# Kernel optimization log

Hardware: AMD Instinct MI355X
Metric: run time of the kernel (lower is better)

Reference implementation:

```python
import jax, jax.numpy as jnp
import numpy as np

N_NODES = 100000
N_EDGES = 3200000
N_PAIRS = 500000
D_IN = 256
D_HID = 256
D_OUT = 2


def setup_inputs() -> dict:
    key = jax.random.key(0)
    ks = jax.random.split(key, 9)
    s1 = 1.0 / np.sqrt(D_IN)
    s2 = 1.0 / np.sqrt(D_HID)
    s3 = 1.0 / np.sqrt(2 * D_HID)
    return {
        "x": jax.random.normal(ks[0], (N_NODES, D_IN), jnp.float32),
        "edge_index": jax.random.randint(ks[1], (2, N_EDGES), 0, N_NODES, jnp.int64 if jax.config.jax_enable_x64 else jnp.int32),
        "index": jax.random.randint(ks[2], (N_PAIRS, 2), 0, N_NODES, jnp.int64 if jax.config.jax_enable_x64 else jnp.int32),
        "W1": jax.random.normal(ks[3], (D_HID, D_IN), jnp.float32) * s1,
        "b1": jnp.zeros((D_HID,), jnp.float32),
        "W2": jax.random.normal(ks[4], (D_HID, D_HID), jnp.float32) * s2,
        "b2": jnp.zeros((D_HID,), jnp.float32),
        "W3": jax.random.normal(ks[5], (D_OUT, 2 * D_HID), jnp.float32) * s3,
        "b3": jnp.zeros((D_OUT,), jnp.float32),
    }


def _gin_conv(x, edge_index, W, b):
    # PyG GINConv (eps=0): nn((1+eps)*x + sum_{j in N(i)} x_j)
    src, dst = edge_index[0], edge_index[1]
    agg = jax.ops.segment_sum(x[src], dst, num_segments=x.shape[0])  # [N, d]
    return (x + agg) @ W.T + b


def reference(x, edge_index, index, W1, b1, W2, b2, W3, b3):
    h = jax.nn.relu(_gin_conv(x, edge_index, W1, b1))   # [N, D_HID]
    h = jax.nn.relu(_gin_conv(h, edge_index, W2, b2))   # [N, D_HID]
    pair = jnp.concatenate((h[index[:, 0]], h[index[:, 1]]), axis=-1)  # [P, 2*D_HID]
    logits = pair @ W3.T + b3                            # [P, D_OUT]
    return jax.nn.log_softmax(logits, axis=1)
```

## Files before the change

### kernel.cpp

```cpp
#include <hip/hip_runtime.h>
#include <hip/hip_bf16.h>

constexpr int N_NODES = 100000;
constexpr int N_EDGES = 3200000;
constexpr int N_PAIRS = 500000;
constexpr int D       = 256;

using frag_ab = __attribute__((ext_vector_type(8))) short;
using frag_cd = __attribute__((ext_vector_type(4))) float;
typedef unsigned short ushort8 __attribute__((ext_vector_type(8)));

static __device__ __forceinline__ float b2f(unsigned short u) {
  return __uint_as_float(((unsigned)u) << 16);
}
static __device__ __forceinline__ unsigned short f2bf(float f) {
  unsigned u = __float_as_uint(f);
  unsigned r = (u + 0x7fff + ((u >> 16) & 1)) >> 16;
  return (unsigned short)r;
}

__global__ void zero_ints(int* __restrict__ p, int n) {
  int i = blockIdx.x * blockDim.x + threadIdx.x;
  if (i < n) p[i] = 0;
}

__global__ void f32_to_bf16(const float4* __restrict__ in, ushort4* __restrict__ out, int n4) {
  int i = blockIdx.x * blockDim.x + threadIdx.x;
  int stride = gridDim.x * blockDim.x;
  for (; i < n4; i += stride) {
    const float4 v = in[i];
    ushort4 o;
    o.x = f2bf(v.x); o.y = f2bf(v.y); o.z = f2bf(v.z); o.w = f2bf(v.w);
    out[i] = o;
  }
}

__global__ void hist_kernel(const int* __restrict__ ei, int* __restrict__ counts) {
  int i = blockIdx.x * blockDim.x + threadIdx.x;
  if (i < N_EDGES) atomicAdd(&counts[ei[N_EDGES + i]], 1);
}

__global__ __launch_bounds__(1024) void scan_kernel(const int* __restrict__ counts,
                                                    int* __restrict__ cursor, int n) {
  __shared__ int wsum[16];
  __shared__ int carry;
  const int t = threadIdx.x, lane = t & 63, w = t >> 6;
  if (t == 0) carry = 0;
  __syncthreads();
  for (int base = 0; base < n; base += 1024) {
    int v = (base + t < n) ? counts[base + t] : 0;
    int s = v;
#pragma unroll
    for (int off = 1; off < 64; off <<= 1) {
      int u = __shfl_up(s, off, 64);
      if (lane >= off) s += u;
    }
    if (lane == 63) wsum[w] = s;
    __syncthreads();
    if (t < 16) {
      int ws = wsum[t];
#pragma unroll
      for (int off = 1; off < 16; off <<= 1) {
        int u = __shfl_up(ws, off, 64);
        if (lane >= off) ws += u;
      }
      wsum[t] = ws;
    }
    __syncthreads();
    const int wpre = (w == 0) ? 0 : wsum[w - 1];
    if (base + t < n) cursor[base + t] = carry + wpre + s - v;
    __syncthreads();
    if (t == 0) carry += wsum[15];
    __syncthreads();
  }
}

constexpr int FILL_SEG = 4096;
__global__ __launch_bounds__(256) void fill_kernel(const int* __restrict__ ei,
                                                   int* __restrict__ cursor,
                                                   int* __restrict__ csr) {
  const int range = blockIdx.x & 7;
  const int seg   = blockIdx.x >> 3;
  const int base  = seg * FILL_SEG;
  const int lo = range * 12500, hi = lo + 12500;
#pragma unroll
  for (int j = 0; j < FILL_SEG / 256; ++j) {
    const int i = base + j * 256 + threadIdx.x;
    if (i < N_EDGES) {
      const int dst = ei[N_EDGES + i];
      if (dst >= lo && dst < hi) {
        const int pos = atomicAdd(&cursor[dst], 1);
        csr[pos] = ei[i];
      }
    }
  }
}

__global__ __launch_bounds__(256) void gather_agg_bf16(const ushort* __restrict__ x,
                                                       const int* __restrict__ csr,
                                                       const int* __restrict__ cursor_end,
                                                       const int* __restrict__ counts,
                                                       ushort* __restrict__ out) {
  const int node = blockIdx.x * 4 + (threadIdx.x >> 6);
  const int lane = threadIdx.x & 63;
  const int half = lane >> 5;
  const int fl   = lane & 31;
  if (node >= N_NODES) return;
  const int end = cursor_end[node];
  const int beg = end - counts[node];
  const size_t fo = (size_t)fl * 8;

  float acc[8];
#pragma unroll
  for (int j = 0; j < 8; ++j) acc[j] = 0.f;

  if (half == 0) {
    const ushort8 self = *reinterpret_cast<const ushort8*>(x + (size_t)node * D + fo);
#pragma unroll
    for (int j = 0; j < 8; ++j) acc[j] += b2f(self[j]);
  }

  int o = beg + half;
  for (; o + 6 < end; o += 8) {
    const int s0 = csr[o], s1 = csr[o + 2], s2 = csr[o + 4], s3 = csr[o + 6];
    const ushort8 v0 = *reinterpret_cast<const ushort8*>(x + (size_t)s0 * D + fo);
    const ushort8 v1 = *reinterpret_cast<const ushort8*>(x + (size_t)s1 * D + fo);
    const ushort8 v2 = *reinterpret_cast<const ushort8*>(x + (size_t)s2 * D + fo);
    const ushort8 v3 = *reinterpret_cast<const ushort8*>(x + (size_t)s3 * D + fo);
#pragma unroll
    for (int j = 0; j < 8; ++j)
      acc[j] += (b2f(v0[j]) + b2f(v1[j])) + (b2f(v2[j]) + b2f(v3[j]));
  }
  for (; o < end; o += 2) {
    const ushort8 v = *reinterpret_cast<const ushort8*>(x + (size_t)csr[o] * D + fo);
#pragma unroll
    for (int j = 0; j < 8; ++j) acc[j] += b2f(v[j]);
  }

#pragma unroll
  for (int j = 0; j < 8; ++j) acc[j] += __shfl_xor(acc[j], 32, 64);

  if (half == 0) {
    ushort8 ov;
#pragma unroll
    for (int j = 0; j < 8; ++j) ov[j] = f2bf(acc[j]);
    *reinterpret_cast<ushort8*>(out + (size_t)node * D + fo) = ov;
  }
}

__global__ __launch_bounds__(256) void gemm_mfma_bf16(const ushort* __restrict__ A,
                                                      const ushort* __restrict__ W,
                                                      const float* __restrict__ bias,
                                                      ushort* __restrict__ C,
                                                      int M) {
  __shared__ __align__(16) ushort As[64 * 256];
  __shared__ __align__(16) ushort Ws[64 * 256];

  const int t = threadIdx.x;
  const int w = t >> 6, l = t & 63;
  const int row0 = blockIdx.x * 64;
  const int col0 = blockIdx.y * 64;

  {
    const float4 zero4 = {0.f, 0.f, 0.f, 0.f};
#pragma unroll
    for (int i = 0; i < 8; ++i) {
      const int chunk = t + i * 256;
      const int r  = chunk >> 5;
      const int kb = (chunk & 31) << 4;
      const int swz = kb ^ ((r & 7) << 4);
      const int grow = row0 + r;
      float4 av = zero4;
      if (grow < M)
        av = *reinterpret_cast<const float4*>(
            reinterpret_cast<const char*>(A) + (size_t)grow * 512 + kb);
      *reinterpret_cast<float4*>(reinterpret_cast<char*>(As) + r * 512 + swz) = av;
      const float4 wv = *reinterpret_cast<const float4*>(
          reinterpret_cast<const char*>(W) + (size_t)(col0 + r) * 512 + kb);
      *reinterpret_cast<float4*>(reinterpret_cast<char*>(Ws) + r * 512 + swz) = wv;
    }
  }
  __syncthreads();

  const int g  = l >> 4;
  const int fr = l & 15;

  frag_cd acc[4];
#pragma unroll
  for (int c = 0; c < 4; ++c) {
    acc[c][0] = 0.f; acc[c][1] = 0.f; acc[c][2] = 0.f; acc[c][3] = 0.f;
  }

  const int arow = w * 16 + fr;
  const char* Asb = reinterpret_cast<const char*>(As);
  const char* Wsb = reinterpret_cast<const char*>(Ws);
#pragma unroll
  for (int ks = 0; ks < 8; ++ks) {
    const int kb = ks * 64 + g * 16;
    const frag_ab af = *reinterpret_cast<const frag_ab*>(
        Asb + arow * 512 + (kb ^ ((arow & 7) << 4)));
#pragma unroll
    for (int c = 0; c < 4; ++c) {
      const int wrow = c * 16 + fr;
      const frag_ab bf = *reinterpret_cast<const frag_ab*>(
          Wsb + wrow * 512 + (kb ^ ((wrow & 7) << 4)));
      acc[c] = __builtin_amdgcn_mfma_f32_16x16x32_bf16(af, bf, acc[c], 0, 0, 0);
    }
  }
  __syncthreads();

  ushort* Ct = As;
#pragma unroll
  for (int c = 0; c < 4; ++c) {
    const int col = c * 16 + fr;
    const float bv = bias[col0 + col];
#pragma unroll
    for (int r = 0; r < 4; ++r) {
      const int rl = w * 16 + g * 4 + r;
      Ct[rl * 64 + col] = f2bf(fmaxf(acc[c][r] + bv, 0.f));
    }
  }
  __syncthreads();
#pragma unroll
  for (int i = 0; i < 2; ++i) {
    const int chunk = t + i * 256;
    const int r  = chunk >> 3;
    const int cb = (chunk & 7) << 4;
    const int grow = row0 + r;
    if (grow < M)
      *reinterpret_cast<float4*>(reinterpret_cast<char*>(C) + (size_t)grow * 512 + col0 * 2 + cb) =
          *reinterpret_cast<const float4*>(reinterpret_cast<const char*>(Ct) + r * 128 + cb);
  }
}

__global__ __launch_bounds__(256) void pair_head_bf16(const ushort* __restrict__ h,
                                                      const int* __restrict__ idx,
                                                      const float* __restrict__ W3,
                                                      const float* __restrict__ b3,
                                                      float* __restrict__ out) {
  const int wave = (int)((blockIdx.x * (size_t)blockDim.x + threadIdx.x) >> 6);
  const int lane = threadIdx.x & 63;
  const int half = lane >> 5;
  const int fl   = lane & 31;
  const int p0 = 2 * wave, p1 = 2 * wave + 1;
  if (p0 >= N_PAIRS) return;

  const int ia = idx[2 * p0 + half];
  const int ib = idx[2 * p1 + half];
  const ushort8 va = *reinterpret_cast<const ushort8*>(h + (size_t)ia * D + fl * 8);
  const ushort8 vb = *reinterpret_cast<const ushort8*>(h + (size_t)ib * D + fl * 8);

  const float4 w0a = *reinterpret_cast<const float4*>(W3 + lane * 8);
  const float4 w0b = *reinterpret_cast<const float4*>(W3 + lane * 8 + 4);
  const float4 w1a = *reinterpret_cast<const float4*>(W3 + 512 + lane * 8);
  const float4 w1b = *reinterpret_cast<const float4*>(W3 + 512 + lane * 8 + 4);
  const float w0[8] = {w0a.x, w0a.y, w0a.z, w0a.w, w0b.x, w0b.y, w0b.z, w0b.w};
  const float w1[8] = {w1a.x, w1a.y, w1a.z, w1a.w, w1b.x, w1b.y, w1b.z, w1b.w};

  float l00 = 0.f, l01 = 0.f, l10 = 0.f, l11 = 0.f;
#pragma unroll
  for (int j = 0; j < 8; ++j) {
    const float fa = b2f(va[j]), fb = b2f(vb[j]);
    l00 += fa * w0[j]; l01 += fa * w1[j];
    l10 += fb * w0[j]; l11 += fb * w1[j];
  }
#pragma unroll
  for (int off = 32; off > 0; off >>= 1) {
    l00 += __shfl_down(l00, off, 64);
    l01 += __shfl_down(l01, off, 64);
    l10 += __shfl_down(l10, off, 64);
    l11 += __shfl_down(l11, off, 64);
  }
  if (lane == 0) {
    const float bb0 = b3[0], bb1 = b3[1];
    l00 += bb0; l01 += bb1; l10 += bb0; l11 += bb1;
    const float m0 = fmaxf(l00, l01);
    const float lse0 = m0 + logf(expf(l00 - m0) + expf(l01 - m0));
    const float m1 = fmaxf(l10, l11);
    const float lse1 = m1 + logf(expf(l10 - m1) + expf(l11 - m1));
    float4 o;
    o.x = l00 - lse0; o.y = l01 - lse0; o.z = l10 - lse1; o.w = l11 - lse1;
    *reinterpret_cast<float4*>(out + 4 * (size_t)wave) = o;
  }
}

extern "C" void kernel_launch(void* const* d_in, const int* in_sizes, int n_in,
                              void* d_out, int out_size, void* d_ws, size_t ws_size,
                              hipStream_t stream) {
  const float* x   = (const float*)d_in[0];
  const int*   ei  = (const int*)d_in[1];
  const int*   idx = (const int*)d_in[2];
  const float* W1  = (const float*)d_in[3];
  const float* b1  = (const float*)d_in[4];
  const float* W2  = (const float*)d_in[5];
  const float* b2  = (const float*)d_in[6];
  const float* W3  = (const float*)d_in[7];
  const float* b3  = (const float*)d_in[8];
  float* out = (float*)d_out;

  const size_t feat = (size_t)N_NODES * D;
  char* ws = (char*)d_ws;
  ushort* xb    = (ushort*)(ws);
  ushort* aggb  = (ushort*)(ws + 51200000);
  ushort* hb    = (ushort*)(ws + 102400000);
  ushort* W1b   = (ushort*)(ws + 153600000);
  ushort* W2b   = (ushort*)(ws + 153731072);
  int* counts   = (int*)(ws + 153862144);
  int* cursor   = (int*)(ws + 154262144);
  int* csr      = (int*)(ws + 154662144);

  const dim3 blk(256);
  const dim3 zeroGrid((N_NODES + 255) / 256);
  const dim3 edgeGrid((N_EDGES + 255) / 256);
  const int  nseg = (N_EDGES + FILL_SEG - 1) / FILL_SEG;
  const dim3 fillGrid(8 * nseg);
  const dim3 nodeGrid((N_NODES + 3) / 4);
  const dim3 gemmGrid((N_NODES + 63) / 64, D / 64);
  const dim3 pairGrid(((size_t)(N_PAIRS / 2) * 64 + 255) / 256);

  f32_to_bf16<<<dim3(4096), blk, 0, stream>>>((const float4*)x, (ushort4*)xb, (int)(feat / 4));
  f32_to_bf16<<<dim3(64), blk, 0, stream>>>((const float4*)W1, (ushort4*)W1b, 65536 / 4);
  f32_to_bf16<<<dim3(64), blk, 0, stream>>>((const float4*)W2, (ushort4*)W2b, 65536 / 4);

  zero_ints<<<zeroGrid, blk, 0, stream>>>(counts, N_NODES);
  hist_kernel<<<edgeGrid, blk, 0, stream>>>(ei, counts);
  scan_kernel<<<1, 1024, 0, stream>>>(counts, cursor, N_NODES);
  fill_kernel<<<fillGrid, blk, 0, stream>>>(ei, cursor, csr);

  gather_agg_bf16<<<nodeGrid, blk, 0, stream>>>(xb, csr, cursor, counts, aggb);
  gemm_mfma_bf16<<<gemmGrid, blk, 0, stream>>>(aggb, W1b, b1, hb, N_NODES);

  gather_agg_bf16<<<nodeGrid, blk, 0, stream>>>(hb, csr, cursor, counts, aggb);
  gemm_mfma_bf16<<<gemmGrid, blk, 0, stream>>>(aggb, W2b, b2, hb, N_NODES);

  pair_head_bf16<<<pairGrid, blk, 0, stream>>>(hb, idx, W3, b3, out);
}
```

Baseline: 1.035 ms.

## Bucket CSR neighbor lists by source chunk to improve gather locality

Builds a per-destination, per-source-chunk histogram (16 chunks) so each node's neighbor list in the CSR is partially sorted by source index range. The gather kernels then touch source feature rows in a more localized order, aiming for better L2/cache hit rates during aggregation. This adds a larger histogram, extra rowsum and chunk-position kernels, and more scattered atomics in the CSR build. The scratch space it uses overlaps the hidden-feature buffer, which is only written later.

```diff
diff --git a/kernel.cpp b/kernel.cpp
--- a/kernel.cpp
+++ b/kernel.cpp
@@ -5,6 +5,8 @@
 constexpr int N_EDGES = 3200000;
 constexpr int N_PAIRS = 500000;
 constexpr int D       = 256;
+constexpr int NCHUNK  = 16;
+constexpr int CHUNK_NODES = N_NODES / NCHUNK;
 
 using frag_ab = __attribute__((ext_vector_type(8))) short;
 using frag_cd = __attribute__((ext_vector_type(4))) float;
@@ -35,9 +37,39 @@
   }
 }
 
-__global__ void hist_kernel(const int* __restrict__ ei, int* __restrict__ counts) {
+__global__ void hist2_kernel(const int* __restrict__ ei, int* __restrict__ cnt2) {
   int i = blockIdx.x * blockDim.x + threadIdx.x;
-  if (i < N_EDGES) atomicAdd(&counts[ei[N_EDGES + i]], 1);
+  if (i < N_EDGES) {
+    const int src = ei[i];
+    const int dst = ei[N_EDGES + i];
+    atomicAdd(&cnt2[dst * NCHUNK + src / CHUNK_NODES], 1);
+  }
+}
+
+__global__ void rowsum_kernel(const int* __restrict__ cnt2, int* __restrict__ counts) {
+  const int node = blockIdx.x * blockDim.x + threadIdx.x;
+  if (node >= N_NODES) return;
+  const int4* r = reinterpret_cast<const int4*>(cnt2 + node * NCHUNK);
+  int s = 0;
+#pragma unroll
+  for (int j = 0; j < NCHUNK / 4; ++j) {
+    const int4 v = r[j];
+    s += v.x + v.y + v.z + v.w;
+  }
+  counts[node] = s;
+}
+
+__global__ void chunkpos_kernel(const int* __restrict__ cnt2, const int* __restrict__ cursor,
+                                int* __restrict__ pos2) {
+  const int node = blockIdx.x * blockDim.x + threadIdx.x;
+  if (node >= N_NODES) return;
+  int run = cursor[node];
+#pragma unroll
+  for (int c = 0; c < NCHUNK; ++c) {
+    const int v = cnt2[node * NCHUNK + c];
+    pos2[node * NCHUNK + c] = run;
+    run += v;
+  }
 }
 
 __global__ __launch_bounds__(1024) void scan_kernel(const int* __restrict__ counts,
@@ -76,9 +108,9 @@
 }
 
 constexpr int FILL_SEG = 4096;
-__global__ __launch_bounds__(256) void fill_kernel(const int* __restrict__ ei,
-                                                   int* __restrict__ cursor,
-                                                   int* __restrict__ csr) {
+__global__ __launch_bounds__(256) void fill2_kernel(const int* __restrict__ ei,
+                                                    int* __restrict__ pos2,
+                                                    int* __restrict__ csr) {
   const int range = blockIdx.x & 7;
   const int seg   = blockIdx.x >> 3;
   const int base  = seg * FILL_SEG;
@@ -89,8 +121,9 @@
     if (i < N_EDGES) {
       const int dst = ei[N_EDGES + i];
       if (dst >= lo && dst < hi) {
-        const int pos = atomicAdd(&cursor[dst], 1);
-        csr[pos] = ei[i];
+        const int src = ei[i];
+        const int pos = atomicAdd(&pos2[dst * NCHUNK + src / CHUNK_NODES], 1);
+        csr[pos] = src;
       }
     }
   }
@@ -98,7 +131,7 @@
 
 __global__ __launch_bounds__(256) void gather_agg_bf16(const ushort* __restrict__ x,
                                                        const int* __restrict__ csr,
-                                                       const int* __restrict__ cursor_end,
+                                                       const int* __restrict__ cursor,
                                                        const int* __restrict__ counts,
                                                        ushort* __restrict__ out) {
   const int node = blockIdx.x * 4 + (threadIdx.x >> 6);
@@ -106,8 +139,8 @@
   const int half = lane >> 5;
   const int fl   = lane & 31;
   if (node >= N_NODES) return;
-  const int end = cursor_end[node];
-  const int beg = end - counts[node];
+  const int beg = cursor[node];
+  const int end = beg + counts[node];
   const size_t fo = (size_t)fl * 8;
 
   float acc[8];
@@ -303,6 +336,8 @@
   ushort* xb    = (ushort*)(ws);
   ushort* aggb  = (ushort*)(ws + 51200000);
   ushort* hb    = (ushort*)(ws + 102400000);
+  int* cnt2     = (int*)(ws + 102400000);
+  int* pos2     = (int*)(ws + 102400000 + 6400000);
   ushort* W1b   = (ushort*)(ws + 153600000);
   ushort* W2b   = (ushort*)(ws + 153731072);
   int* counts   = (int*)(ws + 153862144);
@@ -310,7 +345,8 @@
   int* csr      = (int*)(ws + 154662144);
 
   const dim3 blk(256);
-  const dim3 zeroGrid((N_NODES + 255) / 256);
+  const dim3 cnt2Grid((N_NODES * NCHUNK + 255) / 256);
+  const dim3 nodeThreadGrid((N_NODES + 255) / 256);
   const dim3 edgeGrid((N_EDGES + 255) / 256);
   const int  nseg = (N_EDGES + FILL_SEG - 1) / FILL_SEG;
   const dim3 fillGrid(8 * nseg);
@@ -322,10 +358,12 @@
   f32_to_bf16<<<dim3(64), blk, 0, stream>>>((const float4*)W1, (ushort4*)W1b, 65536 / 4);
   f32_to_bf16<<<dim3(64), blk, 0, stream>>>((const float4*)W2, (ushort4*)W2b, 65536 / 4);
 
-  zero_ints<<<zeroGrid, blk, 0, stream>>>(counts, N_NODES);
-  hist_kernel<<<edgeGrid, blk, 0, stream>>>(ei, counts);
+  zero_ints<<<cnt2Grid, blk, 0, stream>>>(cnt2, N_NODES * NCHUNK);
+  hist2_kernel<<<edgeGrid, blk, 0, stream>>>(ei, cnt2);
+  rowsum_kernel<<<nodeThreadGrid, blk, 0, stream>>>(cnt2, counts);
   scan_kernel<<<1, 1024, 0, stream>>>(counts, cursor, N_NODES);
-  fill_kernel<<<fillGrid, blk, 0, stream>>>(ei, cursor, csr);
+  chunkpos_kernel<<<nodeThreadGrid, blk, 0, stream>>>(cnt2, cursor, pos2);
+  fill2_kernel<<<fillGrid, blk, 0, stream>>>(ei, pos2, csr);
 
   gather_agg_bf16<<<nodeGrid, blk, 0, stream>>>(xb, csr, cursor, counts, aggb);
   gemm_mfma_bf16<<<gemmGrid, blk, 0, stream>>>(aggb, W1b, b1, hb, N_NODES);
```

New measurement: 1.037 ms. Within noise of the previous version (+0.2%).

## Gather aggregation in source-chunk phases with register accumulators and grid sync

Applied to the files above, without the earlier changes.

Builds a CSR sorted by (source chunk, destination) so each wave owns 49 destination nodes kept as register accumulators, then sweeps 16 source-node chunks in lockstep. A cooperative grid sync between chunks keeps all waves reading the same slice of the feature matrix, so the gathered rows should stay resident in cache. Edge indices are preloaded into registers and broadcast with shuffles. The cost is a larger multi-kernel scan, heavy register pressure from 49 float4 accumulators, a fixed grid of 512 blocks, and 16 grid-wide barriers per layer.

```diff
diff --git a/kernel.cpp b/kernel.cpp
--- a/kernel.cpp
+++ b/kernel.cpp
@@ -1,10 +1,20 @@
 #include <hip/hip_runtime.h>
 #include <hip/hip_bf16.h>
+#include <hip/hip_cooperative_groups.h>
+
+namespace cg = cooperative_groups;
 
 constexpr int N_NODES = 100000;
 constexpr int N_EDGES = 3200000;
 constexpr int N_PAIRS = 500000;
 constexpr int D       = 256;
+constexpr int NCHUNK  = 16;
+constexpr int CHUNK_NODES = N_NODES / NCHUNK;
+constexpr int GATHER_BLOCKS = 512;
+constexpr int N_WAVES = GATHER_BLOCKS * 4;
+constexpr int NPW     = 49;
+constexpr int NPAD    = N_WAVES * NPW;
+constexpr int SEGN    = NCHUNK * NPAD;
 
 using frag_ab = __attribute__((ext_vector_type(8))) short;
 using frag_cd = __attribute__((ext_vector_type(4))) float;
@@ -35,9 +45,43 @@
   }
 }
 
-__global__ void hist_kernel(const int* __restrict__ ei, int* __restrict__ counts) {
+__global__ void hist_cm_kernel(const int* __restrict__ ei, int* __restrict__ cnt) {
   int i = blockIdx.x * blockDim.x + threadIdx.x;
-  if (i < N_EDGES) atomicAdd(&counts[ei[N_EDGES + i]], 1);
+  if (i < N_EDGES) {
+    const int src = ei[i];
+    const int dst = ei[N_EDGES + i];
+    atomicAdd(&cnt[(src / CHUNK_NODES) * NPAD + dst], 1);
+  }
+}
+
+__global__ __launch_bounds__(1024) void scan_block_k(const int* __restrict__ in,
+                                                     int* __restrict__ out,
+                                                     int* __restrict__ bsum) {
+  __shared__ int wsum[16];
+  const int t = threadIdx.x, lane = t & 63, w = t >> 6;
+  const int gid = blockIdx.x * 1024 + t;
+  const int v = in[gid];
+  int s = v;
+#pragma unroll
+  for (int off = 1; off < 64; off <<= 1) {
+    int u = __shfl_up(s, off, 64);
+    if (lane >= off) s += u;
+  }
+  if (lane == 63) wsum[w] = s;
+  __syncthreads();
+  if (t < 16) {
+    int ws = wsum[t];
+#pragma unroll
+    for (int off = 1; off < 16; off <<= 1) {
+      int u = __shfl_up(ws, off, 64);
+      if (lane >= off) ws += u;
+    }
+    wsum[t] = ws;
+  }
+  __syncthreads();
+  const int wpre = (w == 0) ? 0 : wsum[w - 1];
+  out[gid] = wpre + s - v;
+  if (t == 1023) bsum[blockIdx.x] = wsum[15];
 }
 
 __global__ __launch_bounds__(1024) void scan_kernel(const int* __restrict__ counts,
@@ -75,10 +119,17 @@
   }
 }
 
+__global__ __launch_bounds__(1024) void scan_add_k(int* __restrict__ p2s,
+                                                   const int* __restrict__ bsum2) {
+  const int gid = blockIdx.x * 1024 + threadIdx.x;
+  p2s[gid] += bsum2[gid >> 10];
+  if (gid == 0) p2s[SEGN] = N_EDGES;
+}
+
 constexpr int FILL_SEG = 4096;
-__global__ __launch_bounds__(256) void fill_kernel(const int* __restrict__ ei,
-                                                   int* __restrict__ cursor,
-                                                   int* __restrict__ csr) {
+__global__ __launch_bounds__(256) void fill_cm_kernel(const int* __restrict__ ei,
+                                                      int* __restrict__ pos,
+                                                      int* __restrict__ csr) {
   const int range = blockIdx.x & 7;
   const int seg   = blockIdx.x >> 3;
   const int base  = seg * FILL_SEG;
@@ -89,62 +140,88 @@
     if (i < N_EDGES) {
       const int dst = ei[N_EDGES + i];
       if (dst >= lo && dst < hi) {
-        const int pos = atomicAdd(&cursor[dst], 1);
-        csr[pos] = ei[i];
+        const int src = ei[i];
+        const int p = atomicAdd(&pos[(src / CHUNK_NODES) * NPAD + dst], 1);
+        csr[p] = src;
       }
     }
   }
 }
 
-__global__ __launch_bounds__(256) void gather_agg_bf16(const ushort* __restrict__ x,
-                                                       const int* __restrict__ csr,
-                                                       const int* __restrict__ cursor_end,
-                                                       const int* __restrict__ counts,
-                                                       ushort* __restrict__ out) {
-  const int node = blockIdx.x * 4 + (threadIdx.x >> 6);
+template <bool SYNC>
+__global__ __launch_bounds__(256, 2) void gather_phased(const ushort* __restrict__ x,
+                                                        const int* __restrict__ csr,
+                                                        const int* __restrict__ p2s,
+                                                        ushort* __restrict__ out) {
+  const int wave = blockIdx.x * 4 + (threadIdx.x >> 6);
   const int lane = threadIdx.x & 63;
-  const int half = lane >> 5;
-  const int fl   = lane & 31;
-  if (node >= N_NODES) return;
-  const int end = cursor_end[node];
-  const int beg = end - counts[node];
-  const size_t fo = (size_t)fl * 8;
-
-  float acc[8];
-#pragma unroll
-  for (int j = 0; j < 8; ++j) acc[j] = 0.f;
-
-  if (half == 0) {
-    const ushort8 self = *reinterpret_cast<const ushort8*>(x + (size_t)node * D + fo);
-#pragma unroll
-    for (int j = 0; j < 8; ++j) acc[j] += b2f(self[j]);
-  }
-
-  int o = beg + half;
-  for (; o + 6 < end; o += 8) {
-    const int s0 = csr[o], s1 = csr[o + 2], s2 = csr[o + 4], s3 = csr[o + 6];
-    const ushort8 v0 = *reinterpret_cast<const ushort8*>(x + (size_t)s0 * D + fo);
-    const ushort8 v1 = *reinterpret_cast<const ushort8*>(x + (size_t)s1 * D + fo);
-    const ushort8 v2 = *reinterpret_cast<const ushort8*>(x + (size_t)s2 * D + fo);
-    const ushort8 v3 = *reinterpret_cast<const ushort8*>(x + (size_t)s3 * D + fo);
-#pragma unroll
-    for (int j = 0; j < 8; ++j)
-      acc[j] += (b2f(v0[j]) + b2f(v1[j])) + (b2f(v2[j]) + b2f(v3[j]));
-  }
-  for (; o < end; o += 2) {
-    const ushort8 v = *reinterpret_cast<const ushort8*>(x + (size_t)csr[o] * D + fo);
-#pragma unroll
-    for (int j = 0; j < 8; ++j) acc[j] += b2f(v[j]);
-  }
-
-#pragma unroll
-  for (int j = 0; j < 8; ++j) acc[j] += __shfl_xor(acc[j], 32, 64);
-
-  if (half == 0) {
-    ushort8 ov;
-#pragma unroll
-    for (int j = 0; j < 8; ++j) ov[j] = f2bf(acc[j]);
-    *reinterpret_cast<ushort8*>(out + (size_t)node * D + fo) = ov;
+  const int n0 = wave * NPW;
+
+  float4 acc[NPW];
+#pragma unroll
+  for (int i = 0; i < NPW; ++i) {
+    const int node = n0 + i;
+    if (node < N_NODES) {
+      const ushort4 v = *reinterpret_cast<const ushort4*>(x + (size_t)node * D + lane * 4);
+      acc[i].x = b2f(v.x); acc[i].y = b2f(v.y); acc[i].z = b2f(v.z); acc[i].w = b2f(v.w);
+    } else {
+      acc[i].x = acc[i].y = acc[i].z = acc[i].w = 0.f;
+    }
+  }
+
+  for (int c = 0; c < NCHUNK; ++c) {
+    const int li = (lane <= NPW) ? lane : NPW;
+    const int segv = p2s[c * NPAD + n0 + li];
+    const int base = __shfl(segv, 0, 64);
+    const int wend = __shfl(segv, NPW, 64);
+    const int nE = wend - base;
+    const int e0 = (lane      < nE) ? csr[base + lane]       : 0;
+    const int e1 = (lane + 64 < nE) ? csr[base + lane + 64]  : 0;
+    const int e2 = (lane + 128 < nE) ? csr[base + lane + 128] : 0;
+
+#pragma unroll
+    for (int i = 0; i < NPW; ++i) {
+      const int s = __shfl(segv, i, 64);
+      const int e = __shfl(segv, i + 1, 64);
+      int o = s;
+      while (o + 1 < e) {
+        const int k0 = o - base, k1 = k0 + 1;
+        int i0, i1;
+        if (k1 < 192) {
+          i0 = (k0 < 64) ? __shfl(e0, k0, 64) : (k0 < 128) ? __shfl(e1, k0 & 63, 64) : __shfl(e2, k0 & 63, 64);
+          i1 = (k1 < 64) ? __shfl(e0, k1, 64) : (k1 < 128) ? __shfl(e1, k1 & 63, 64) : __shfl(e2, k1 & 63, 64);
+        } else { i0 = csr[o]; i1 = csr[o + 1]; }
+        const ushort4 v0 = *reinterpret_cast<const ushort4*>(x + (size_t)i0 * D + lane * 4);
+        const ushort4 v1 = *reinterpret_cast<const ushort4*>(x + (size_t)i1 * D + lane * 4);
+        acc[i].x += b2f(v0.x) + b2f(v1.x);
+        acc[i].y += b2f(v0.y) + b2f(v1.y);
+        acc[i].z += b2f(v0.z) + b2f(v1.z);
+        acc[i].w += b2f(v0.w) + b2f(v1.w);
+        o += 2;
+      }
+      if (o < e) {
+        const int k = o - base;
+        int is;
+        if (k < 192) {
+          is = (k < 64) ? __shfl(e0, k, 64) : (k < 128) ? __shfl(e1, k & 63, 64) : __shfl(e2, k & 63, 64);
+        } else is = csr[o];
+        const ushort4 v = *reinterpret_cast<const ushort4*>(x + (size_t)is * D + lane * 4);
+        acc[i].x += b2f(v.x); acc[i].y += b2f(v.y); acc[i].z += b2f(v.z); acc[i].w += b2f(v.w);
+      }
+    }
+    if constexpr (SYNC) {
+      if (c + 1 < NCHUNK) cg::this_grid().sync();
+    }
+  }
+
+#pragma unroll
+  for (int i = 0; i < NPW; ++i) {
+    const int node = n0 + i;
+    if (node < N_NODES) {
+      ushort4 ov;
+      ov.x = f2bf(acc[i].x); ov.y = f2bf(acc[i].y); ov.z = f2bf(acc[i].z); ov.w = f2bf(acc[i].w);
+      *reinterpret_cast<ushort4*>(out + (size_t)node * D + lane * 4) = ov;
+    }
   }
 }
 
@@ -298,40 +375,60 @@
   const float* b3  = (const float*)d_in[8];
   float* out = (float*)d_out;
 
+  char* ws = (char*)d_ws;
+  ushort* buf0 = (ushort*)(ws);
+  ushort* buf1 = (ushort*)(ws + 51200000);
+  ushort* W1b  = (ushort*)(ws + 102400000);
+  ushort* W2b  = (ushort*)(ws + 102531072);
+  int* p2s     = (int*)(ws + 102662144);
+  int* csr     = (int*)(ws + 109084800);
+  int* cnt     = (int*)(ws + 51200000);
+  int* pos     = (int*)(ws + 51200000 + 8000000);
+  int* bsum    = (int*)(ws + 51200000 + 16000000);
+  int* bsum2   = (int*)(ws + 51200000 + 16100000);
+
+  const dim3 blk(256);
   const size_t feat = (size_t)N_NODES * D;
-  char* ws = (char*)d_ws;
-  ushort* xb    = (ushort*)(ws);
-  ushort* aggb  = (ushort*)(ws + 51200000);
-  ushort* hb    = (ushort*)(ws + 102400000);
-  ushort* W1b   = (ushort*)(ws + 153600000);
-  ushort* W2b   = (ushort*)(ws + 153731072);
-  int* counts   = (int*)(ws + 153862144);
-  int* cursor   = (int*)(ws + 154262144);
-  int* csr      = (int*)(ws + 154662144);
-
-  const dim3 blk(256);
-  const dim3 zeroGrid((N_NODES + 255) / 256);
   const dim3 edgeGrid((N_EDGES + 255) / 256);
   const int  nseg = (N_EDGES + FILL_SEG - 1) / FILL_SEG;
   const dim3 fillGrid(8 * nseg);
-  const dim3 nodeGrid((N_NODES + 3) / 4);
   const dim3 gemmGrid((N_NODES + 63) / 64, D / 64);
   const dim3 pairGrid(((size_t)(N_PAIRS / 2) * 64 + 255) / 256);
-
-  f32_to_bf16<<<dim3(4096), blk, 0, stream>>>((const float4*)x, (ushort4*)xb, (int)(feat / 4));
+  constexpr int SCAN_BLOCKS = SEGN / 1024;
+
+  f32_to_bf16<<<dim3(4096), blk, 0, stream>>>((const float4*)x, (ushort4*)buf0, (int)(feat / 4));
   f32_to_bf16<<<dim3(64), blk, 0, stream>>>((const float4*)W1, (ushort4*)W1b, 65536 / 4);
   f32_to_bf16<<<dim3(64), blk, 0, stream>>>((const float4*)W2, (ushort4*)W2b, 65536 / 4);
 
-  zero_ints<<<zeroGrid, blk, 0, stream>>>(counts, N_NODES);
-  hist_kernel<<<edgeGrid, blk, 0, stream>>>(ei, counts);
-  scan_kernel<<<1, 1024, 0, stream>>>(counts, cursor, N_NODES);
-  fill_kernel<<<fillGrid, blk, 0, stream>>>(ei, cursor, csr);
-
-  gather_agg_bf16<<<nodeGrid, blk, 0, stream>>>(xb, csr, cursor, counts, aggb);
-  gemm_mfma_bf16<<<gemmGrid, blk, 0, stream>>>(aggb, W1b, b1, hb, N_NODES);
-
-  gather_agg_bf16<<<nodeGrid, blk, 0, stream>>>(hb, csr, cursor, counts, aggb);
-  gemm_mfma_bf16<<<gemmGrid, blk, 0, stream>>>(aggb, W2b, b2, hb, N_NODES);
-
-  pair_head_bf16<<<pairGrid, blk, 0, stream>>>(hb, idx, W3, b3, out);
-}
+  zero_ints<<<dim3((SEGN + 255) / 256), blk, 0, stream>>>(cnt, SEGN);
+  hist_cm_kernel<<<edgeGrid, blk, 0, stream>>>(ei, cnt);
+  scan_block_k<<<dim3(SCAN_BLOCKS), dim3(1024), 0, stream>>>(cnt, p2s, bsum);
+  scan_kernel<<<1, 1024, 0, stream>>>(bsum, bsum2, SCAN_BLOCKS);
+  scan_add_k<<<dim3(SCAN_BLOCKS), dim3(1024), 0, stream>>>(p2s, bsum2);
+  hipMemcpyAsync(pos, p2s, (size_t)SEGN * 4, hipMemcpyDeviceToDevice, stream);
+  fill_cm_kernel<<<fillGrid, blk, 0, stream>>>(ei, pos, csr);
+
+  int maxb = 0;
+  hipError_t qe = hipOccupancyMaxActiveBlocksPerMultiprocessor(&maxb, gather_phased<true>, 256, 0);
+  const bool coop_ok = (qe == hipSuccess) && (maxb >= 2);
+
+  auto launch_gather = [&](const ushort* in, ushort* o) {
+    if (coop_ok) {
+      const ushort* a0 = in; const int* a1 = csr; const int* a2 = p2s; ushort* a3 = o;
+      void* args[] = {(void*)&a0, (void*)&a1, (void*)&a2, (void*)&a3};
+      hipError_t le = hipLaunchCooperativeKernel(gather_phased<true>,
+                                                 dim3(GATHER_BLOCKS), dim3(256),
+                                                 args, 0, stream);
+      if (le == hipSuccess) return;
+    }
+    gather_phased<false><<<dim3(GATHER_BLOCKS), blk, 0, stream>>>(in, csr, p2s, o);
+  };
+
+  launch_gather(buf0, buf1);
+  gemm_mfma_bf16<<<gemmGrid, blk, 0, stream>>>(buf1, W1b, b1, buf0, N_NODES);
+
+  launch_gather(buf0, buf1);
+  gemm_mfma_bf16<<<gemmGrid, blk, 0, stream>>>(buf1, W2b, b2, buf0, N_NODES);
+
+  pair_head_bf16<<<pairGrid, blk, 0, stream>>>(buf0, idx, W3, b3, out);
+}
```

Measured after the change: 1.581 ms. +52.8%, slower.

## Precompute per-node W3 projections and make pair head a tiny gather

Applied to the files above, without the earlier changes.

The final linear layer is split per node, so each node's hidden vector is projected once onto both halves of W3, storing four floats per node. The pair kernel then gathers two 16-byte projections per pair, adds the bias and applies log-softmax. This replaces the large per-pair gathers of full 256-wide rows. It adds an extra kernel and a copy of the scan offsets so the fill kernel no longer overwrites the start positions.

```diff
diff --git a/kernel.cpp b/kernel.cpp
--- a/kernel.cpp
+++ b/kernel.cpp
@@ -22,6 +22,11 @@
 __global__ void zero_ints(int* __restrict__ p, int n) {
   int i = blockIdx.x * blockDim.x + threadIdx.x;
   if (i < n) p[i] = 0;
+}
+
+__global__ void copy_ints(const int* __restrict__ in, int* __restrict__ out, int n) {
+  int i = blockIdx.x * blockDim.x + threadIdx.x;
+  if (i < n) out[i] = in[i];
 }
 
 __global__ void f32_to_bf16(const float4* __restrict__ in, ushort4* __restrict__ out, int n4) {
@@ -77,7 +82,7 @@
 
 constexpr int FILL_SEG = 4096;
 __global__ __launch_bounds__(256) void fill_kernel(const int* __restrict__ ei,
-                                                   int* __restrict__ cursor,
+                                                   int* __restrict__ pos,
                                                    int* __restrict__ csr) {
   const int range = blockIdx.x & 7;
   const int seg   = blockIdx.x >> 3;
@@ -89,8 +94,8 @@
     if (i < N_EDGES) {
       const int dst = ei[N_EDGES + i];
       if (dst >= lo && dst < hi) {
-        const int pos = atomicAdd(&cursor[dst], 1);
-        csr[pos] = ei[i];
+        const int p = atomicAdd(&pos[dst], 1);
+        csr[p] = ei[i];
       }
     }
   }
@@ -98,7 +103,7 @@
 
 __global__ __launch_bounds__(256) void gather_agg_bf16(const ushort* __restrict__ x,
                                                        const int* __restrict__ csr,
-                                                       const int* __restrict__ cursor_end,
+                                                       const int* __restrict__ cursor,
                                                        const int* __restrict__ counts,
                                                        ushort* __restrict__ out) {
   const int node = blockIdx.x * 4 + (threadIdx.x >> 6);
@@ -106,8 +111,8 @@
   const int half = lane >> 5;
   const int fl   = lane & 31;
   if (node >= N_NODES) return;
-  const int end = cursor_end[node];
-  const int beg = end - counts[node];
+  const int beg = cursor[node];
+  const int end = beg + counts[node];
   const size_t fo = (size_t)fl * 8;
 
   float acc[8];
@@ -233,55 +238,54 @@
   }
 }
 
-__global__ __launch_bounds__(256) void pair_head_bf16(const ushort* __restrict__ h,
-                                                      const int* __restrict__ idx,
-                                                      const float* __restrict__ W3,
-                                                      const float* __restrict__ b3,
-                                                      float* __restrict__ out) {
-  const int wave = (int)((blockIdx.x * (size_t)blockDim.x + threadIdx.x) >> 6);
+__global__ __launch_bounds__(256) void proj_kernel(const ushort* __restrict__ h,
+                                                   const float* __restrict__ W3,
+                                                   float4* __restrict__ proj) {
+  const int node = blockIdx.x * 4 + (threadIdx.x >> 6);
   const int lane = threadIdx.x & 63;
-  const int half = lane >> 5;
-  const int fl   = lane & 31;
-  const int p0 = 2 * wave, p1 = 2 * wave + 1;
-  if (p0 >= N_PAIRS) return;
-
-  const int ia = idx[2 * p0 + half];
-  const int ib = idx[2 * p1 + half];
-  const ushort8 va = *reinterpret_cast<const ushort8*>(h + (size_t)ia * D + fl * 8);
-  const ushort8 vb = *reinterpret_cast<const ushort8*>(h + (size_t)ib * D + fl * 8);
-
-  const float4 w0a = *reinterpret_cast<const float4*>(W3 + lane * 8);
-  const float4 w0b = *reinterpret_cast<const float4*>(W3 + lane * 8 + 4);
-  const float4 w1a = *reinterpret_cast<const float4*>(W3 + 512 + lane * 8);
-  const float4 w1b = *reinterpret_cast<const float4*>(W3 + 512 + lane * 8 + 4);
-  const float w0[8] = {w0a.x, w0a.y, w0a.z, w0a.w, w0b.x, w0b.y, w0b.z, w0b.w};
-  const float w1[8] = {w1a.x, w1a.y, w1a.z, w1a.w, w1b.x, w1b.y, w1b.z, w1b.w};
-
-  float l00 = 0.f, l01 = 0.f, l10 = 0.f, l11 = 0.f;
-#pragma unroll
-  for (int j = 0; j < 8; ++j) {
-    const float fa = b2f(va[j]), fb = b2f(vb[j]);
-    l00 += fa * w0[j]; l01 += fa * w1[j];
-    l10 += fb * w0[j]; l11 += fb * w1[j];
-  }
+  if (node >= N_NODES) return;
+
+  const ushort4 hv = *reinterpret_cast<const ushort4*>(h + (size_t)node * D + lane * 4);
+  const float h0 = b2f(hv.x), h1 = b2f(hv.y), h2 = b2f(hv.z), h3 = b2f(hv.w);
+
+  const float4 wa0 = *reinterpret_cast<const float4*>(W3 + lane * 4);
+  const float4 wa1 = *reinterpret_cast<const float4*>(W3 + 512 + lane * 4);
+  const float4 wb0 = *reinterpret_cast<const float4*>(W3 + 256 + lane * 4);
+  const float4 wb1 = *reinterpret_cast<const float4*>(W3 + 768 + lane * 4);
+
+  float a0 = h0 * wa0.x + h1 * wa0.y + h2 * wa0.z + h3 * wa0.w;
+  float a1 = h0 * wa1.x + h1 * wa1.y + h2 * wa1.z + h3 * wa1.w;
+  float b0 = h0 * wb0.x + h1 * wb0.y + h2 * wb0.z + h3 * wb0.w;
+  float b1 = h0 * wb1.x + h1 * wb1.y + h2 * wb1.z + h3 * wb1.w;
+
 #pragma unroll
   for (int off = 32; off > 0; off >>= 1) {
-    l00 += __shfl_down(l00, off, 64);
-    l01 += __shfl_down(l01, off, 64);
-    l10 += __shfl_down(l10, off, 64);
-    l11 += __shfl_down(l11, off, 64);
+    a0 += __shfl_xor(a0, off, 64);
+    a1 += __shfl_xor(a1, off, 64);
+    b0 += __shfl_xor(b0, off, 64);
+    b1 += __shfl_xor(b1, off, 64);
   }
   if (lane == 0) {
-    const float bb0 = b3[0], bb1 = b3[1];
-    l00 += bb0; l01 += bb1; l10 += bb0; l11 += bb1;
-    const float m0 = fmaxf(l00, l01);
-    const float lse0 = m0 + logf(expf(l00 - m0) + expf(l01 - m0));
-    const float m1 = fmaxf(l10, l11);
-    const float lse1 = m1 + logf(expf(l10 - m1) + expf(l11 - m1));
-    float4 o;
-    o.x = l00 - lse0; o.y = l01 - lse0; o.z = l10 - lse1; o.w = l11 - lse1;
-    *reinterpret_cast<float4*>(out + 4 * (size_t)wave) = o;
-  }
+    float4 o; o.x = a0; o.y = a1; o.z = b0; o.w = b1;
+    proj[node] = o;
+  }
+}
+
+__global__ __launch_bounds__(256) void pair_lite(const float4* __restrict__ proj,
+                                                 const int* __restrict__ idx,
+                                                 const float* __restrict__ b3,
+                                                 float* __restrict__ out) {
+  const int p = blockIdx.x * blockDim.x + threadIdx.x;
+  if (p >= N_PAIRS) return;
+  const int2 ii = reinterpret_cast<const int2*>(idx)[p];
+  const float4 pa = proj[ii.x];
+  const float4 pb = proj[ii.y];
+  float l0 = pa.x + pb.z + b3[0];
+  float l1 = pa.y + pb.w + b3[1];
+  const float m = fmaxf(l0, l1);
+  const float lse = m + logf(expf(l0 - m) + expf(l1 - m));
+  float2 o; o.x = l0 - lse; o.y = l1 - lse;
+  reinterpret_cast<float2*>(out)[p] = o;
 }
 
 extern "C" void kernel_launch(void* const* d_in, const int* in_sizes, int n_in,
@@ -298,7 +302,6 @@
   const float* b3  = (const float*)d_in[8];
   float* out = (float*)d_out;
 
-  const size_t feat = (size_t)N_NODES * D;
   char* ws = (char*)d_ws;
   ushort* xb    = (ushort*)(ws);
   ushort* aggb  = (ushort*)(ws + 51200000);
@@ -307,16 +310,19 @@
   ushort* W2b   = (ushort*)(ws + 153731072);
   int* counts   = (int*)(ws + 153862144);
   int* cursor   = (int*)(ws + 154262144);
-  int* csr      = (int*)(ws + 154662144);
+  int* pos      = (int*)(ws + 154662144);
+  int* csr      = (int*)(ws + 155062144);
+  float4* proj  = (float4*)(ws + 167862144);
 
   const dim3 blk(256);
+  const size_t feat = (size_t)N_NODES * D;
   const dim3 zeroGrid((N_NODES + 255) / 256);
   const dim3 edgeGrid((N_EDGES + 255) / 256);
   const int  nseg = (N_EDGES + FILL_SEG - 1) / FILL_SEG;
   const dim3 fillGrid(8 * nseg);
   const dim3 nodeGrid((N_NODES + 3) / 4);
   const dim3 gemmGrid((N_NODES + 63) / 64, D / 64);
-  const dim3 pairGrid(((size_t)(N_PAIRS / 2) * 64 + 255) / 256);
+  const dim3 pairGrid((N_PAIRS + 255) / 256);
 
   f32_to_bf16<<<dim3(4096), blk, 0, stream>>>((const float4*)x, (ushort4*)xb, (int)(feat / 4));
   f32_to_bf16<<<dim3(64), blk, 0, stream>>>((const float4*)W1, (ushort4*)W1b, 65536 / 4);
@@ -325,7 +331,8 @@
   zero_ints<<<zeroGrid, blk, 0, stream>>>(counts, N_NODES);
   hist_kernel<<<edgeGrid, blk, 0, stream>>>(ei, counts);
   scan_kernel<<<1, 1024, 0, stream>>>(counts, cursor, N_NODES);
-  fill_kernel<<<fillGrid, blk, 0, stream>>>(ei, cursor, csr);
+  copy_ints<<<zeroGrid, blk, 0, stream>>>(cursor, pos, N_NODES);
+  fill_kernel<<<fillGrid, blk, 0, stream>>>(ei, pos, csr);
 
   gather_agg_bf16<<<nodeGrid, blk, 0, stream>>>(xb, csr, cursor, counts, aggb);
   gemm_mfma_bf16<<<gemmGrid, blk, 0, stream>>>(aggb, W1b, b1, hb, N_NODES);
@@ -333,5 +340,6 @@
   gather_agg_bf16<<<nodeGrid, blk, 0, stream>>>(hb, csr, cursor, counts, aggb);
   gemm_mfma_bf16<<<gemmGrid, blk, 0, stream>>>(aggb, W2b, b2, hb, N_NODES);
 
-  pair_head_bf16<<<pairGrid, blk, 0, stream>>>(hb, idx, W3, b3, out);
-}
+  proj_kernel<<<nodeGrid, blk, 0, stream>>>(hb, W3, proj);
+  pair_lite<<<pairGrid, blk, 0, stream>>>(proj, idx, b3, out);
+}
```

Result: faster. 990.8 us (-4.2%).
